# Optimization experiments

Hardware: AMD Instinct MI355X
Metric: run time of the kernel (lower is better)

The kernel has to match this reference:

```python
import jax, jax.numpy as jnp
import numpy as np

N = 100000          # nodes
E = 1600000         # edges (avg degree 16)
D_IN = 128          # in_features
D_OUT = 128         # out_features


def setup_inputs() -> dict:
    key = jax.random.key(0)
    k1, k2, k3, k4 = jax.random.split(key, 4)
    H = jax.random.normal(k1, (N, D_IN), dtype=jnp.float32)
    # COO indices of sparse adjacency A: row i aggregates features of col j
    src = jax.random.randint(k2, (E,), 0, N, dtype=jnp.int32)
    dst = jax.random.randint(k3, (E,), 0, N, dtype=jnp.int32)
    # nn.Linear(2*in_features, out_features): weight [out, 2*in], zero bias
    W = jax.random.normal(k4, (D_OUT, 2 * D_IN), dtype=jnp.float32) * 0.05
    b = jnp.zeros((D_OUT,), dtype=jnp.float32)
    return {"H": H, "src": src, "dst": dst, "W": W, "b": b}


def reference(H, src, dst, W, b):
    # max-aggregation: for each node i, max over features of its neighbors.
    # One fused gather + segment-max replaces the per-node Python loop.
    gathered = H[dst]  # [E, D_IN]
    agg = jax.ops.segment_max(gathered, src, num_segments=N)  # [N, D_IN]
    # nodes with no incoming edges stay zero (torch code leaves zeros)
    deg = jax.ops.segment_sum(jnp.ones((src.shape[0],), jnp.float32), src,
                              num_segments=N)  # [N]
    H_neigh = jnp.where(deg[:, None] > 0, agg, 0.0)
    H_concat = jnp.concatenate([H, H_neigh], axis=1)  # [N, 2*D_IN]
    return H_concat @ W.T + b
```

## Files before the change

### kernel.cpp

```cpp
#include <hip/hip_runtime.h>
#include <math.h>

#define NN 100000
#define NE 1600000
#define DD 128
#define NB 1563
#define CAP 1280
#define PB 196
#define CB 196

#define WS_HH  0
#define WS_CUR 6400000
#define WS_ENT (WS_CUR + NB)
#define WS_AH  (WS_ENT + NB * CAP)

typedef __attribute__((ext_vector_type(8))) _Float16 h8_t;
typedef __attribute__((ext_vector_type(2))) _Float16 h2_t;
typedef __attribute__((ext_vector_type(4))) float f4_t;

__device__ __forceinline__ unsigned pk2h(float x, float y) {
    h2_t h;
    h.x = (_Float16)x;
    h.y = (_Float16)y;
    return *(unsigned*)&h;
}

__device__ __forceinline__ h2_t h2max(h2_t a, h2_t b) {
    return __builtin_elementwise_max(a, b);
}

__global__ __launch_bounds__(1024) void cursor_init_kernel(int* __restrict__ cursor) {
    int i = blockIdx.x * 1024 + threadIdx.x;
    if (i < NB) cursor[i] = i * CAP;
}

__global__ __launch_bounds__(1024) void prep_kernel(const float* __restrict__ H,
                                                    const int* __restrict__ src,
                                                    const int* __restrict__ dst,
                                                    int* __restrict__ cursor,
                                                    unsigned* __restrict__ entries,
                                                    uint4* __restrict__ Hh4) {
    __shared__ int cnt[NB];
    __shared__ int gcur[NB];
    const int t = threadIdx.x;
    const int b = blockIdx.x;
    if (b < PB) {
        for (int i = t; i < NB; i += 1024) cnt[i] = 0;
        __syncthreads();
        const int base = b * 8192;
        int sv[8];
#pragma unroll
        for (int k = 0; k < 8; ++k) {
            int e = base + k * 1024 + t;
            sv[k] = (e < NE) ? src[e] : -1;
            if (sv[k] >= 0) atomicAdd(&cnt[sv[k] >> 6], 1);
        }
        __syncthreads();
        for (int i = t; i < NB; i += 1024) {
            int c = cnt[i];
            gcur[i] = c ? atomicAdd(&cursor[i], c) : 0;
        }
        __syncthreads();
#pragma unroll
        for (int k = 0; k < 8; ++k) {
            int e = base + k * 1024 + t;
            if (sv[k] >= 0) {
                int s = sv[k];
                int pos = atomicAdd(&gcur[s >> 6], 1);
                entries[pos] = ((unsigned)(s & 63) << 17) | (unsigned)dst[e];
            }
        }
    } else {
        const int nb = b - PB;
        const int n8 = NN * DD / 8;
        for (int i = nb * 1024 + t; i < n8; i += CB * 1024) {
            const float4* s = (const float4*)H + (size_t)i * 2;
            float4 a = s[0], c4 = s[1];
            uint4 o;
            o.x = pk2h(a.x, a.y);
            o.y = pk2h(a.z, a.w);
            o.z = pk2h(c4.x, c4.y);
            o.w = pk2h(c4.z, c4.w);
            Hh4[i] = o;
        }
    }
}

__global__ __launch_bounds__(256) void agg_kernel(const _Float16* __restrict__ Hh,
                                                  const int* __restrict__ cursor,
                                                  const unsigned* __restrict__ entries,
                                                  unsigned* __restrict__ Ah) {
    __shared__ unsigned raw[CAP];
    __shared__ unsigned sorted[CAP];
    __shared__ int cnt[64], base_s[64], cur[64];
    const int t = threadIdx.x;
    const int b = blockIdx.x;
    const int n = cursor[b] - b * CAP;

    if (t < 64) cnt[t] = 0;
    __syncthreads();
    for (int i = t; i < n; i += 256) {
        unsigned e = entries[b * CAP + i];
        raw[i] = e;
        atomicAdd(&cnt[e >> 17], 1);
    }
    __syncthreads();
    if (t < 64) {
        int v = cnt[t];
        int incl = v;
#pragma unroll
        for (int o = 1; o < 64; o <<= 1) {
            int y = __shfl_up(incl, o, 64);
            if (t >= o) incl += y;
        }
        base_s[t] = incl - v;
        cur[t] = incl - v;
    }
    __syncthreads();
    for (int i = t; i < n; i += 256) {
        unsigned e = raw[i];
        int pos = atomicAdd(&cur[e >> 17], 1);
        sorted[pos] = e & 0x1FFFFu;
    }
    __syncthreads();

    const int lane = t & 63;
    const int w = t >> 6;
#pragma unroll
    for (int q = 0; q < 16; ++q) {
        int ln = w * 16 + q;
        int s0 = base_s[ln];
        int e0 = s0 + cnt[ln];
        unsigned mu = 0xFC00FC00u;
        h2_t m = *(h2_t*)&mu;
        int j = s0;
        for (; j + 4 <= e0; j += 4) {
            unsigned d0 = sorted[j], d1 = sorted[j + 1];
            unsigned d2 = sorted[j + 2], d3 = sorted[j + 3];
            h2_t v0 = *(const h2_t*)(Hh + (size_t)d0 * DD + lane * 2);
            h2_t v1 = *(const h2_t*)(Hh + (size_t)d1 * DD + lane * 2);
            h2_t v2 = *(const h2_t*)(Hh + (size_t)d2 * DD + lane * 2);
            h2_t v3 = *(const h2_t*)(Hh + (size_t)d3 * DD + lane * 2);
            m = h2max(m, h2max(h2max(v0, v1), h2max(v2, v3)));
        }
        for (; j < e0; ++j) {
            h2_t v0 = *(const h2_t*)(Hh + (size_t)sorted[j] * DD + lane * 2);
            m = h2max(m, v0);
        }
        int node = b * 64 + ln;
        if (node < NN) {
            unsigned outv = (s0 < e0) ? *(unsigned*)&m : 0u;
            Ah[(size_t)node * 64 + lane] = outv;
        }
    }
}

#define XP 72
__global__ __launch_bounds__(256) void mfma_matmul_kernel(
        const unsigned short* __restrict__ Hh,
        const unsigned short* __restrict__ Ah,
        const float* __restrict__ W,
        const float* __restrict__ bias,
        float* __restrict__ out) {
    __shared__ unsigned short Xs[64 * XP];
    __shared__ unsigned short Ws[128 * XP];
    const int t = threadIdx.x;
    const int lane = t & 63;
    const int w = t >> 6;
    const int quad = lane >> 4;
    const int l16 = lane & 15;
    const int blockrow = blockIdx.x * 64;

    f4_t acc[8] = {};

    for (int c = 0; c < 4; ++c) {
        const int k0 = c * 64;
        {
            const unsigned short* xb = (c < 2) ? Hh : Ah;
            const int koff = (c < 2) ? k0 : k0 - 128;
            int seg = t & 7, r0 = t >> 3;
#pragma unroll
            for (int j = 0; j < 2; ++j) {
                int r = r0 + 32 * j;
                int row = blockrow + r;
                uint4 v = make_uint4(0, 0, 0, 0);
                if (row < NN)
                    v = *(const uint4*)(xb + (size_t)row * DD + koff + seg * 8);
                *(uint4*)&Xs[r * XP + seg * 8] = v;
            }
        }
        {
            int seg = t & 15, o0 = t >> 4;
#pragma unroll
            for (int j = 0; j < 8; ++j) {
                int o = o0 + 16 * j;
                float4 wv = *(const float4*)(W + (size_t)o * 256 + k0 + seg * 4);
                uint2 p;
                p.x = pk2h(wv.x, wv.y);
                p.y = pk2h(wv.z, wv.w);
                *(uint2*)&Ws[o * XP + seg * 4] = p;
            }
        }
        __syncthreads();
#pragma unroll
        for (int kk = 0; kk < 64; kk += 32) {
            h8_t a = *(const h8_t*)&Xs[(w * 16 + l16) * XP + kk + quad * 8];
#pragma unroll
            for (int ot = 0; ot < 8; ++ot) {
                h8_t bf = *(const h8_t*)&Ws[(ot * 16 + l16) * XP + kk + quad * 8];
                acc[ot] = __builtin_amdgcn_mfma_f32_16x16x32_f16(a, bf, acc[ot], 0, 0, 0);
            }
        }
        __syncthreads();
    }

#pragma unroll
    for (int ot = 0; ot < 8; ++ot) {
        float bv = bias[ot * 16 + l16];
#pragma unroll
        for (int reg = 0; reg < 4; ++reg) {
            int row = blockrow + w * 16 + quad * 4 + reg;
            if (row < NN)
                out[(size_t)row * DD + ot * 16 + l16] = acc[ot][reg] + bv;
        }
    }
}

extern "C" void kernel_launch(void* const* d_in, const int* in_sizes, int n_in,
                              void* d_out, int out_size, void* d_ws, size_t ws_size,
                              hipStream_t stream) {
    const float* H   = (const float*)d_in[0];
    const int*   src = (const int*)d_in[1];
    const int*   dst = (const int*)d_in[2];
    const float* W   = (const float*)d_in[3];
    const float* b   = (const float*)d_in[4];
    float* out = (float*)d_out;

    int* ws = (int*)d_ws;
    unsigned short* Hh      = (unsigned short*)(ws + WS_HH);
    int*            cursor  = ws + WS_CUR;
    unsigned*       entries = (unsigned*)(ws + WS_ENT);
    unsigned*       Ah      = (unsigned*)(ws + WS_AH);

    cursor_init_kernel<<<2, 1024, 0, stream>>>(cursor);
    prep_kernel<<<PB + CB, 1024, 0, stream>>>(H, src, dst, cursor, entries, (uint4*)Hh);
    agg_kernel<<<NB, 256, 0, stream>>>((const _Float16*)Hh, cursor, entries, Ah);
    mfma_matmul_kernel<<<(NN + 63) / 64, 256, 0, stream>>>(
        Hh, (const unsigned short*)Ah, W, b, out);
}
```

Measured before the change: 239.8 us.

## Widen agg gathers to 8-byte half4 with split-wave edges, resize prep blocks

The aggregation kernel now has each half-wave handle alternate edges, with lanes loading 4 halves (8 bytes) per neighbour row instead of 2. The two halves are combined with a cross-lane shuffle-xor max, and only the first half writes the result. This is meant to raise memory-level parallelism and cut the instruction count per gathered row. The prep kernel moves to 512-thread blocks with twice as many blocks, and the cursor init kernel is replaced by a memset with relative offsets, saving one launch.

```diff
diff --git a/kernel.cpp b/kernel.cpp
--- a/kernel.cpp
+++ b/kernel.cpp
@@ -6,8 +6,8 @@
 #define DD 128
 #define NB 1563
 #define CAP 1280
-#define PB 196
-#define CB 196
+#define PB 391
+#define CB 391
 
 #define WS_HH  0
 #define WS_CUR 6400000
@@ -15,6 +15,7 @@
 #define WS_AH  (WS_ENT + NB * CAP)
 
 typedef __attribute__((ext_vector_type(8))) _Float16 h8_t;
+typedef __attribute__((ext_vector_type(4))) _Float16 h4_t;
 typedef __attribute__((ext_vector_type(2))) _Float16 h2_t;
 typedef __attribute__((ext_vector_type(4))) float f4_t;
 
@@ -25,45 +26,40 @@
     return *(unsigned*)&h;
 }
 
-__device__ __forceinline__ h2_t h2max(h2_t a, h2_t b) {
+__device__ __forceinline__ h4_t h4max(h4_t a, h4_t b) {
     return __builtin_elementwise_max(a, b);
 }
 
-__global__ __launch_bounds__(1024) void cursor_init_kernel(int* __restrict__ cursor) {
-    int i = blockIdx.x * 1024 + threadIdx.x;
-    if (i < NB) cursor[i] = i * CAP;
-}
-
-__global__ __launch_bounds__(1024) void prep_kernel(const float* __restrict__ H,
-                                                    const int* __restrict__ src,
-                                                    const int* __restrict__ dst,
-                                                    int* __restrict__ cursor,
-                                                    unsigned* __restrict__ entries,
-                                                    uint4* __restrict__ Hh4) {
+__global__ __launch_bounds__(512) void prep_kernel(const float* __restrict__ H,
+                                                   const int* __restrict__ src,
+                                                   const int* __restrict__ dst,
+                                                   int* __restrict__ cursor,
+                                                   unsigned* __restrict__ entries,
+                                                   uint4* __restrict__ Hh4) {
     __shared__ int cnt[NB];
     __shared__ int gcur[NB];
     const int t = threadIdx.x;
     const int b = blockIdx.x;
     if (b < PB) {
-        for (int i = t; i < NB; i += 1024) cnt[i] = 0;
-        __syncthreads();
-        const int base = b * 8192;
+        for (int i = t; i < NB; i += 512) cnt[i] = 0;
+        __syncthreads();
+        const int base = b * 4096;
         int sv[8];
 #pragma unroll
         for (int k = 0; k < 8; ++k) {
-            int e = base + k * 1024 + t;
+            int e = base + k * 512 + t;
             sv[k] = (e < NE) ? src[e] : -1;
             if (sv[k] >= 0) atomicAdd(&cnt[sv[k] >> 6], 1);
         }
         __syncthreads();
-        for (int i = t; i < NB; i += 1024) {
+        for (int i = t; i < NB; i += 512) {
             int c = cnt[i];
-            gcur[i] = c ? atomicAdd(&cursor[i], c) : 0;
+            gcur[i] = c ? i * CAP + atomicAdd(&cursor[i], c) : 0;
         }
         __syncthreads();
 #pragma unroll
         for (int k = 0; k < 8; ++k) {
-            int e = base + k * 1024 + t;
+            int e = base + k * 512 + t;
             if (sv[k] >= 0) {
                 int s = sv[k];
                 int pos = atomicAdd(&gcur[s >> 6], 1);
@@ -73,7 +69,7 @@
     } else {
         const int nb = b - PB;
         const int n8 = NN * DD / 8;
-        for (int i = nb * 1024 + t; i < n8; i += CB * 1024) {
+        for (int i = nb * 512 + t; i < n8; i += CB * 512) {
             const float4* s = (const float4*)H + (size_t)i * 2;
             float4 a = s[0], c4 = s[1];
             uint4 o;
@@ -95,7 +91,7 @@
     __shared__ int cnt[64], base_s[64], cur[64];
     const int t = threadIdx.x;
     const int b = blockIdx.x;
-    const int n = cursor[b] - b * CAP;
+    const int n = cursor[b];
 
     if (t < 64) cnt[t] = 0;
     __syncthreads();
@@ -126,31 +122,41 @@
 
     const int lane = t & 63;
     const int w = t >> 6;
+    const int half = lane >> 5;
+    const int l32 = lane & 31;
+    const _Float16* __restrict__ colbase = Hh + l32 * 4;
 #pragma unroll
     for (int q = 0; q < 16; ++q) {
         int ln = w * 16 + q;
         int s0 = base_s[ln];
         int e0 = s0 + cnt[ln];
-        unsigned mu = 0xFC00FC00u;
-        h2_t m = *(h2_t*)&mu;
-        int j = s0;
-        for (; j + 4 <= e0; j += 4) {
-            unsigned d0 = sorted[j], d1 = sorted[j + 1];
-            unsigned d2 = sorted[j + 2], d3 = sorted[j + 3];
-            h2_t v0 = *(const h2_t*)(Hh + (size_t)d0 * DD + lane * 2);
-            h2_t v1 = *(const h2_t*)(Hh + (size_t)d1 * DD + lane * 2);
-            h2_t v2 = *(const h2_t*)(Hh + (size_t)d2 * DD + lane * 2);
-            h2_t v3 = *(const h2_t*)(Hh + (size_t)d3 * DD + lane * 2);
-            m = h2max(m, h2max(h2max(v0, v1), h2max(v2, v3)));
-        }
-        for (; j < e0; ++j) {
-            h2_t v0 = *(const h2_t*)(Hh + (size_t)sorted[j] * DD + lane * 2);
-            m = h2max(m, v0);
-        }
+        unsigned long long mu = 0xFC00FC00FC00FC00ull;
+        h4_t m = *(h4_t*)&mu;
+        int j = s0 + half;
+        for (; j + 6 < e0; j += 8) {
+            int d0 = sorted[j], d1 = sorted[j + 2];
+            int d2 = sorted[j + 4], d3 = sorted[j + 6];
+            h4_t v0 = *(const h4_t*)(colbase + (size_t)d0 * DD);
+            h4_t v1 = *(const h4_t*)(colbase + (size_t)d1 * DD);
+            h4_t v2 = *(const h4_t*)(colbase + (size_t)d2 * DD);
+            h4_t v3 = *(const h4_t*)(colbase + (size_t)d3 * DD);
+            m = h4max(m, h4max(h4max(v0, v1), h4max(v2, v3)));
+        }
+        for (; j < e0; j += 2) {
+            h4_t v0 = *(const h4_t*)(colbase + (size_t)sorted[j] * DD);
+            m = h4max(m, v0);
+        }
+        uint2 mv = *(uint2*)&m;
+        uint2 ov;
+        ov.x = (unsigned)__shfl_xor((int)mv.x, 32, 64);
+        ov.y = (unsigned)__shfl_xor((int)mv.y, 32, 64);
+        h4_t om = *(h4_t*)&ov;
+        m = h4max(m, om);
         int node = b * 64 + ln;
-        if (node < NN) {
-            unsigned outv = (s0 < e0) ? *(unsigned*)&m : 0u;
-            Ah[(size_t)node * 64 + lane] = outv;
+        if (half == 0 && node < NN) {
+            uint2 outv = make_uint2(0u, 0u);
+            if (s0 < e0) outv = *(uint2*)&m;
+            *(uint2*)(Ah + (size_t)node * 64 + l32 * 2) = outv;
         }
     }
 }
@@ -242,8 +248,8 @@
     unsigned*       entries = (unsigned*)(ws + WS_ENT);
     unsigned*       Ah      = (unsigned*)(ws + WS_AH);
 
-    cursor_init_kernel<<<2, 1024, 0, stream>>>(cursor);
-    prep_kernel<<<PB + CB, 1024, 0, stream>>>(H, src, dst, cursor, entries, (uint4*)Hh);
+    hipMemsetAsync(cursor, 0, NB * sizeof(int), stream);
+    prep_kernel<<<PB + CB, 512, 0, stream>>>(H, src, dst, cursor, entries, (uint4*)Hh);
     agg_kernel<<<NB, 256, 0, stream>>>((const _Float16*)Hh, cursor, entries, Ah);
     mfma_matmul_kernel<<<(NN + 63) / 64, 256, 0, stream>>>(
         Hh, (const unsigned short*)Ah, W, b, out);
```

New measurement: 245.0 us. 1.02x slower.
